# Optimization experiments

Hardware: AMD Instinct MI355X
Metric: run time of the kernel (lower is better)

Reference implementation:

```python
import jax, jax.numpy as jnp
from jax import lax
import numpy as np

K, D, BETA = 512, 64, 0.25

def conv1d(x, w, b=None, stride=1, padding=0):
    # x: [N,C,L], w: [O,I,k] (torch layout)
    y = lax.conv_general_dilated(x, w, (stride,), [(padding, padding)],
                                 dimension_numbers=('NCH', 'OIH', 'NCH'))
    return y if b is None else y + b[None, :, None]

def conv_transpose1d(x, w, b, stride, padding):
    # torch ConvTranspose1d; w: [I,O,k]. Equivalent to dilated conv with flipped, transposed kernel.
    k = w.shape[2]
    wf = jnp.flip(w, 2).transpose(1, 0, 2)  # [O,I,k]
    y = lax.conv_general_dilated(x, wf, (1,), [(k - 1 - padding, k - 1 - padding)],
                                 lhs_dilation=(stride,),
                                 dimension_numbers=('NCH', 'OIH', 'NCH'))
    return y + b[None, :, None]

def residual_stack(x, blocks):
    for w1, w2 in blocks:
        h = conv1d(jax.nn.relu(x), w1, None, 1, 1)
        h = conv1d(jax.nn.relu(h), w2, None, 1, 0)
        x = x + h
    return jax.nn.relu(x)

def setup_inputs() -> dict:
    key = jax.random.key(0)
    ks = iter(jax.random.split(key, 32))
    def w(shape, fan_in):
        return jax.random.normal(next(ks), shape, jnp.float32) / np.sqrt(fan_in)
    H, RH = 128, 32
    inp = {
        'x': jax.random.normal(next(ks), (64, 1, 8192), jnp.float32),
        'ec1_w': w((H // 2, 1, 4), 4), 'ec1_b': jnp.zeros(H // 2, jnp.float32),
        'ec2_w': w((H, H // 2, 4), H // 2 * 4), 'ec2_b': jnp.zeros(H, jnp.float32),
        'ec3_w': w((H, H, 3), H * 3), 'ec3_b': jnp.zeros(H, jnp.float32),
        'er1_w1': w((RH, H, 3), H * 3), 'er1_w2': w((H, RH, 1), RH),
        'er2_w1': w((RH, H, 3), H * 3), 'er2_w2': w((H, RH, 1), RH),
        'pvq_w': w((D, H, 1), H), 'pvq_b': jnp.zeros(D, jnp.float32),
        'codebook': jax.random.uniform(next(ks), (K, D), jnp.float32, -1.0 / K, 1.0 / K),
        'dc1_w': w((H, D, 3), D * 3), 'dc1_b': jnp.zeros(H, jnp.float32),
        'dr1_w1': w((RH, H, 3), H * 3), 'dr1_w2': w((H, RH, 1), RH),
        'dr2_w1': w((RH, H, 3), H * 3), 'dr2_w2': w((H, RH, 1), RH),
        'dt1_w': w((H, H // 2, 4), H * 4), 'dt1_b': jnp.zeros(H // 2, jnp.float32),
        'dt2_w': w((H // 2, 1, 4), H // 2 * 4), 'dt2_b': jnp.zeros(1, jnp.float32),
    }
    return inp

def reference(x, ec1_w, ec1_b, ec2_w, ec2_b, ec3_w, ec3_b,
              er1_w1, er1_w2, er2_w1, er2_w2, pvq_w, pvq_b, codebook,
              dc1_w, dc1_b, dr1_w1, dr1_w2, dr2_w1, dr2_w2,
              dt1_w, dt1_b, dt2_w, dt2_b):
    # ---- Encoder (compression_factor == 4) ----
    h = jax.nn.relu(conv1d(x, ec1_w, ec1_b, 2, 1))
    h = jax.nn.relu(conv1d(h, ec2_w, ec2_b, 2, 1))
    h = conv1d(h, ec3_w, ec3_b, 1, 1)
    h = residual_stack(h, [(er1_w1, er1_w2), (er2_w1, er2_w2)])
    z = conv1d(h, pvq_w, pvq_b, 1, 0)            # [B, D, L/4]

    # ---- Vector quantizer ----
    z_blc = z.transpose(0, 2, 1)                 # [B, L', D]
    flat = z_blc.reshape(-1, D)                  # [N, D]
    dists = (jnp.sum(flat * flat, 1, keepdims=True)
             - 2.0 * flat @ codebook.T
             + jnp.sum(codebook * codebook, 1))  # [N, K]
    idx = jnp.argmin(dists, axis=1)              # [N]
    q = codebook[idx].reshape(z_blc.shape)       # [B, L', D]
    e_latent = jnp.mean((lax.stop_gradient(q) - z_blc) ** 2)
    q_latent = jnp.mean((q - lax.stop_gradient(z_blc)) ** 2)
    vq_loss = q_latent + BETA * e_latent
    q_st = z_blc + lax.stop_gradient(q - z_blc)  # straight-through
    counts = jnp.zeros((K,), z.dtype).at[idx].add(1.0)
    avg_probs = counts / idx.shape[0]
    perplexity = jnp.exp(-jnp.sum(avg_probs * jnp.log(avg_probs + 1e-10)))

    # ---- Decoder (compression_factor == 4) ----
    d = conv1d(q_st.transpose(0, 2, 1), dc1_w, dc1_b, 1, 1)
    d = residual_stack(d, [(dr1_w1, dr1_w2), (dr2_w1, dr2_w2)])
    d = jax.nn.relu(conv_transpose1d(d, dt1_w, dt1_b, 2, 1))
    recon = conv_transpose1d(d, dt2_w, dt2_b, 2, 1)  # [B, 1, L]
    return recon, vq_loss, perplexity
```

## Files before the change

### kernel.cpp

```cpp
#include <hip/hip_runtime.h>
#include <math.h>

static constexpr int NB  = 64;
static constexpr int L0  = 8192;
static constexpr int L1  = 4096;
static constexpr int LQ  = 2048;
static constexpr int CH  = 128;
static constexpr int CHH = 64;
static constexpr int CR  = 32;
static constexpr int CD  = 64;
static constexpr int NK  = 512;
static constexpr int NROWS = NB * LQ;

using short8 = __attribute__((ext_vector_type(8))) short;
using f32x4  = __attribute__((ext_vector_type(4))) float;

__device__ inline f32x4 mfma16(short8 a, short8 b, f32x4 c) {
    return __builtin_amdgcn_mfma_f32_16x16x32_bf16(a, b, c, 0, 0, 0);
}

__device__ inline unsigned short bf16rne(float v) {
    unsigned int bb = __builtin_bit_cast(unsigned int, v);
    unsigned int r = (bb + 0x7FFFu + ((bb >> 16) & 1u)) >> 16;
    return (unsigned short)r;
}
__device__ inline float bf2f(unsigned short s) {
    unsigned int u = ((unsigned int)s) << 16;
    return __builtin_bit_cast(float, u);
}

__global__ __launch_bounds__(256) void k_wtf(const float* __restrict__ src,
                                             short* __restrict__ dst,
                                             int CO, int CI, int K, int iok) {
    int i = blockIdx.x * 256 + threadIdx.x;
    int total = K * CO * CI;
    if (i >= total) return;
    int j  = i & 7;
    int hi = (i >> 3) & 3;
    int cl = (i >> 5) & 15;
    int rest = i >> 9;
    int CIb = CI >> 5, COb = CO >> 4;
    int kb = rest % CIb; rest /= CIb;
    int cb = rest % COb;
    int tap = rest / COb;
    int co = cb * 16 + cl, ci = kb * 32 + hi * 8 + j;
    float v = iok ? src[(ci * CO + co) * K + tap] : src[(co * CI + ci) * K + tap];
    dst[i] = (short)bf16rne(v);
}

__global__ __launch_bounds__(256) void k_w2f(const float* __restrict__ src,
                                             short* __restrict__ hi_dst,
                                             short* __restrict__ lo_dst) {
    int i = blockIdx.x * 256 + threadIdx.x;
    if (i >= CH * CR) return;
    int j  = i & 7;
    int hi = (i >> 3) & 3;
    int cl = (i >> 5) & 15;
    int cb = i >> 9;
    int co = cb * 16 + cl, ci = hi * 8 + j;
    float v = src[co * CR + ci];
    unsigned short h = bf16rne(v);
    hi_dst[i] = (short)h;
    lo_dst[i] = (short)bf16rne(v - bf2f(h));
}

__global__ __launch_bounds__(256) void k_cbf(const float* __restrict__ cb,
                                             short* __restrict__ hi_dst,
                                             short* __restrict__ lo_dst) {
    int i = blockIdx.x * 256 + threadIdx.x;
    if (i >= NK * CD) return;
    int j    = i & 7;
    int l    = (i >> 3) & 63;
    int half = (i >> 9) & 1;
    int mt   = i >> 10;
    int cl = l & 15, hi = l >> 4;
    int m = mt * 16 + cl;
    int k = half * 32 + hi * 8 + j;
    float v = -2.f * cb[m * CD + k];
    unsigned short h = bf16rne(v);
    float r = v - bf2f(h);
    hi_dst[i] = (short)h;
    lo_dst[i] = (short)bf16rne(r);
}

__global__ __launch_bounds__(256) void k_ec1(const float* __restrict__ x,
                                             const float* __restrict__ w,
                                             const float* __restrict__ bias,
                                             float* __restrict__ out) {
    int n = blockIdx.x * 256 + threadIdx.x;
    int t  = n & (L1 - 1);
    int co = (n >> 12) & (CHH - 1);
    int b  = n >> 18;
    const float* xp = x + b * L0;
    float acc = bias[co];
    int p0 = 2 * t - 1;
#pragma unroll
    for (int k = 0; k < 4; ++k) {
        int p = p0 + k;
        if (p >= 0 && p < L0) acc += w[co * 4 + k] * xp[p];
    }
    out[n] = fmaxf(acc, 0.f);
}

template <int CIN, int COUT, int NTAPS, int TSTRIDE, int SWS, int LIN,
          bool RELU_IN, bool TRANS_IN, bool HAS_BIAS, bool RELU_OUT>
__global__ __launch_bounds__(256) void k_mfconv2(const float* __restrict__ x,
                                                 const short* __restrict__ wf,
                                                 const float* __restrict__ bias,
                                                 float* __restrict__ out) {
    constexpr int XW = 63 * TSTRIDE + NTAPS;
    constexpr int MR = (COUT == 128) ? 4 : 1;
    constexpr int COb = COUT / 16, CIb = CIN / 32;
    __shared__ unsigned int xsu[CIN * XW / 2];
    int t0 = blockIdx.x * 64;
    int b  = blockIdx.z;
    int tid = threadIdx.x;

    if (TRANS_IN) {
        for (int i = tid; i < XW * (CIN / 2); i += 256) {
            int j = i / (CIN / 2);
            int ci = (i - j * (CIN / 2)) * 2;
            int p = t0 - 1 + j;
            float vx = 0.f, vy = 0.f;
            if (p >= 0 && p < LIN) {
                const float* s = x + ((size_t)b * LIN + p) * CIN + ci;
                vx = s[0]; vy = s[1];
            }
            if (RELU_IN) { vx = fmaxf(vx, 0.f); vy = fmaxf(vy, 0.f); }
            unsigned int u = (__builtin_bit_cast(unsigned int, vx) >> 16)
                           | (__builtin_bit_cast(unsigned int, vy) & 0xFFFF0000u);
            int byte = (j * CIN + ci) * 2;
            byte ^= ((j >> SWS) & 7) << 4;
            xsu[byte >> 2] = u;
        }
    } else {
        for (int i = tid; i < (CIN / 2) * XW; i += 256) {
            int ci2 = i / XW;
            int j = i - ci2 * XW;
            int ci = ci2 * 2;
            int p = t0 * TSTRIDE - 1 + j;
            float vx = 0.f, vy = 0.f;
            if (p >= 0 && p < LIN) {
                const float* s = x + ((size_t)b * CIN + ci) * LIN + p;
                vx = s[0]; vy = s[LIN];
            }
            if (RELU_IN) { vx = fmaxf(vx, 0.f); vy = fmaxf(vy, 0.f); }
            unsigned int u = (__builtin_bit_cast(unsigned int, vx) >> 16)
                           | (__builtin_bit_cast(unsigned int, vy) & 0xFFFF0000u);
            int byte = (j * CIN + ci) * 2;
            byte ^= ((j >> SWS) & 7) << 4;
            xsu[byte >> 2] = u;
        }
    }
    __syncthreads();

    int l  = tid & 63;
    int w  = tid >> 6;
    int cl = l & 15, hi = l >> 4;
    int co_w = (w & 1) * (MR * 16);
    int t_w  = (w >> 1) * 32;

    f32x4 acc[MR][2];
#pragma unroll
    for (int m = 0; m < MR; ++m)
#pragma unroll
        for (int n = 0; n < 2; ++n) acc[m][n] = (f32x4){0.f, 0.f, 0.f, 0.f};

#pragma unroll
    for (int tap = 0; tap < NTAPS; ++tap) {
#pragma unroll
        for (int kb = 0; kb < CIb; ++kb) {
            const short* ap = wf + ((size_t)((tap * COb + co_w / 16) * CIb + kb)) * 512
                            + cl * 32 + hi * 8;
            short8 a[MR];
#pragma unroll
            for (int m = 0; m < MR; ++m)
                a[m] = *reinterpret_cast<const short8*>(ap + (size_t)m * CIb * 512);
            short8 bf[2];
#pragma unroll
            for (int n = 0; n < 2; ++n) {
                int tt = (t_w + n * 16 + cl) * TSTRIDE + tap;
                int byte = (tt * CIN + kb * 32 + hi * 8) * 2;
                byte ^= ((tt >> SWS) & 7) << 4;
                bf[n] = *reinterpret_cast<const short8*>(
                            reinterpret_cast<const char*>(xsu) + byte);
            }
#pragma unroll
            for (int m = 0; m < MR; ++m)
#pragma unroll
                for (int n = 0; n < 2; ++n)
                    acc[m][n] = mfma16(a[m], bf[n], acc[m][n]);
        }
    }

#pragma unroll
    for (int m = 0; m < MR; ++m) {
#pragma unroll
        for (int n = 0; n < 2; ++n) {
#pragma unroll
            for (int r = 0; r < 4; ++r) {
                int co = co_w + m * 16 + hi * 4 + r;
                int t  = t0 + t_w + n * 16 + cl;
                float v = acc[m][n][r];
                if (HAS_BIAS) v += bias[co];
                if (RELU_OUT) v = fmaxf(v, 0.f);
                out[((size_t)b * COUT + co) * LQ + t] = v;
            }
        }
    }
}

__global__ __launch_bounds__(256) void k_resblk(const float* __restrict__ src,
                                                float* __restrict__ dst,
                                                const short* __restrict__ wf1,
                                                const short* __restrict__ w2h,
                                                const short* __restrict__ w2l) {
    constexpr int XW = 66;
    __shared__ unsigned int xsu[CH * XW / 2];
    __shared__ unsigned int hh[64 * 16];
    __shared__ unsigned int hl[64 * 16];
    int t0 = blockIdx.x * 64;
    int b  = blockIdx.z;
    int tid = threadIdx.x;

    for (int i = tid; i < (CH / 2) * XW; i += 256) {
        int ci2 = i / XW;
        int j = i - ci2 * XW;
        int ci = ci2 * 2;
        int p = t0 - 1 + j;
        float vx = 0.f, vy = 0.f;
        if (p >= 0 && p < LQ) {
            const float* s = src + ((size_t)b * CH + ci) * LQ + p;
            vx = fmaxf(s[0], 0.f); vy = fmaxf(s[LQ], 0.f);
        }
        unsigned int u = (__builtin_bit_cast(unsigned int, vx) >> 16)
                       | (__builtin_bit_cast(unsigned int, vy) & 0xFFFF0000u);
        int byte = (j * CH + ci) * 2;
        byte ^= (j & 7) << 4;
        xsu[byte >> 2] = u;
    }
    __syncthreads();

    int l  = tid & 63;
    int w  = tid >> 6;
    int cl = l & 15, hi = l >> 4;
    int co_w1 = (w & 1) * 16;
    int t_w   = (w >> 1) * 32;

    f32x4 acc1[2];
    acc1[0] = (f32x4){0.f, 0.f, 0.f, 0.f};
    acc1[1] = (f32x4){0.f, 0.f, 0.f, 0.f};
#pragma unroll
    for (int tap = 0; tap < 3; ++tap) {
#pragma unroll
        for (int kb = 0; kb < 4; ++kb) {
            const short* ap = wf1 + ((size_t)((tap * 2 + (w & 1)) * 4 + kb)) * 512
                            + cl * 32 + hi * 8;
            short8 a = *reinterpret_cast<const short8*>(ap);
#pragma unroll
            for (int n = 0; n < 2; ++n) {
                int tt = (t_w + n * 16 + cl) + tap;
                int byte = (tt * CH + kb * 32 + hi * 8) * 2;
                byte ^= (tt & 7) << 4;
                short8 bf = *reinterpret_cast<const short8*>(
                                reinterpret_cast<const char*>(xsu) + byte);
                acc1[n] = mfma16(a, bf, acc1[n]);
            }
        }
    }

#pragma unroll
    for (int n = 0; n < 2; ++n) {
        int t = t_w + n * 16 + cl;
#pragma unroll
        for (int rp = 0; rp < 2; ++rp) {
            float v0 = fmaxf(acc1[n][2 * rp], 0.f);
            float v1 = fmaxf(acc1[n][2 * rp + 1], 0.f);
            unsigned short h0 = bf16rne(v0), h1 = bf16rne(v1);
            unsigned short l0 = bf16rne(v0 - bf2f(h0)), l1 = bf16rne(v1 - bf2f(h1));
            int ciu = (co_w1 >> 1) + hi * 2 + rp;
            int idx = t * 16 + (ciu ^ ((t & 3) << 2));
            hh[idx] = (unsigned int)h0 | ((unsigned int)h1 << 16);
            hl[idx] = (unsigned int)l0 | ((unsigned int)l1 << 16);
        }
    }
    __syncthreads();

    int co2_w = (w & 1) * 64;
    short8 bh[2], bl[2];
#pragma unroll
    for (int n2 = 0; n2 < 2; ++n2) {
        int t = t_w + n2 * 16 + cl;
        int idx = t * 16 + ((hi * 4) ^ ((t & 3) << 2));
        bh[n2] = *reinterpret_cast<const short8*>(&hh[idx]);
        bl[n2] = *reinterpret_cast<const short8*>(&hl[idx]);
    }
#pragma unroll
    for (int m2 = 0; m2 < 4; ++m2) {
        int co2 = co2_w + m2 * 16;
        const short* aph = w2h + (co2 / 16) * 512 + cl * 32 + hi * 8;
        const short* apl = w2l + (co2 / 16) * 512 + cl * 32 + hi * 8;
        short8 ah = *reinterpret_cast<const short8*>(aph);
        short8 al = *reinterpret_cast<const short8*>(apl);
#pragma unroll
        for (int n2 = 0; n2 < 2; ++n2) {
            f32x4 acc = (f32x4){0.f, 0.f, 0.f, 0.f};
            acc = mfma16(ah, bl[n2], acc);
            acc = mfma16(al, bh[n2], acc);
            acc = mfma16(ah, bh[n2], acc);
            int t = t0 + t_w + n2 * 16 + cl;
#pragma unroll
            for (int r = 0; r < 4; ++r) {
                int co = co2 + hi * 4 + r;
                size_t off = ((size_t)b * CH + co) * LQ + t;
                dst[off] = src[off] + acc[r];
            }
        }
    }
}

__global__ __launch_bounds__(256) void k_dt1m(const float* __restrict__ x,
                                              const short* __restrict__ wf,
                                              const float* __restrict__ bias,
                                              float* __restrict__ out) {
    constexpr int XW = 66;
    __shared__ unsigned int xsu[CH * XW / 2];
    int t0 = blockIdx.x * 64;
    int b  = blockIdx.z;
    int tid = threadIdx.x;
    for (int i = tid; i < (CH / 2) * XW; i += 256) {
        int ci2 = i / XW;
        int j = i - ci2 * XW;
        int ci = ci2 * 2;
        int p = t0 - 1 + j;
        float vx = 0.f, vy = 0.f;
        if (p >= 0 && p < LQ) {
            const float* s = x + ((size_t)b * CH + ci) * LQ + p;
            vx = fmaxf(s[0], 0.f); vy = fmaxf(s[LQ], 0.f);
        }
        unsigned int u = (__builtin_bit_cast(unsigned int, vx) >> 16)
                       | (__builtin_bit_cast(unsigned int, vy) & 0xFFFF0000u);
        int byte = (j * CH + ci) * 2;
        byte ^= (j & 7) << 4;
        xsu[byte >> 2] = u;
    }
    __syncthreads();

    int l  = tid & 63;
    int w  = tid >> 6;
    int cl = l & 15, hi = l >> 4;
    int co_w = (w & 1) * 32;
    int u_w  = (w >> 1) * 32;

    f32x4 ae[2][2], ao[2][2];
#pragma unroll
    for (int m = 0; m < 2; ++m)
#pragma unroll
        for (int n = 0; n < 2; ++n) {
            ae[m][n] = (f32x4){0.f, 0.f, 0.f, 0.f};
            ao[m][n] = (f32x4){0.f, 0.f, 0.f, 0.f};
        }

    const int TK[4] = {1, 3, 0, 2};
    const int TO[4] = {1, 0, 2, 1};
#pragma unroll
    for (int te = 0; te < 4; ++te) {
        int k = TK[te], off = TO[te];
#pragma unroll
        for (int kb = 0; kb < 4; ++kb) {
            const short* ap = wf + (size_t)((k * 4 + co_w / 16) * 4 + kb) * 512
                            + cl * 32 + hi * 8;
            short8 a[2];
#pragma unroll
            for (int m = 0; m < 2; ++m)
                a[m] = *reinterpret_cast<const short8*>(ap + (size_t)m * 4 * 512);
            short8 bf[2];
#pragma unroll
            for (int n = 0; n < 2; ++n) {
                int tt = u_w + n * 16 + cl + off;
                int byte = (tt * CH + kb * 32 + hi * 8) * 2;
                byte ^= (tt & 7) << 4;
                bf[n] = *reinterpret_cast<const short8*>(
                            reinterpret_cast<const char*>(xsu) + byte);
            }
#pragma unroll
            for (int m = 0; m < 2; ++m)
#pragma unroll
                for (int n = 0; n < 2; ++n) {
                    if (te < 2) ae[m][n] = mfma16(a[m], bf[n], ae[m][n]);
                    else        ao[m][n] = mfma16(a[m], bf[n], ao[m][n]);
                }
        }
    }

#pragma unroll
    for (int m = 0; m < 2; ++m) {
#pragma unroll
        for (int n = 0; n < 2; ++n) {
#pragma unroll
            for (int r = 0; r < 4; ++r) {
                int co = co_w + m * 16 + hi * 4 + r;
                int u  = t0 + u_w + n * 16 + cl;
                float bv = bias[co];
                float2 rr;
                rr.x = fmaxf(ae[m][n][r] + bv, 0.f);
                rr.y = fmaxf(ao[m][n][r] + bv, 0.f);
                *reinterpret_cast<float2*>(&out[((size_t)b * CHH + co) * L1 + 2 * u]) = rr;
            }
        }
    }
}

__global__ __launch_bounds__(256) void k_pvqr(const float* __restrict__ x,
                                              const float* __restrict__ w,
                                              const float* __restrict__ bias,
                                              float* __restrict__ z) {
    __shared__ float xs[CH][64];
    __shared__ float wT[CH][64];
    int tid = threadIdx.x;
    int t0 = blockIdx.x * 64;
    int b = blockIdx.y;
    for (int i = tid; i < CD * CH; i += 256) {
        int d = i >> 7, ci = i & 127;
        wT[ci][d] = w[i];
    }
    for (int i = tid; i < CH * 64; i += 256) {
        int ci = i >> 6, j = i & 63;
        xs[ci][j] = fmaxf(x[((size_t)b * CH + ci) * LQ + t0 + j], 0.f);
    }
    __syncthreads();
    int d = tid & 63;
    int tg = tid >> 6;
    float bv = bias[d];
    float acc[16];
#pragma unroll
    for (int i = 0; i < 16; ++i) acc[i] = bv;
    for (int ci = 0; ci < CH; ++ci) {
        float wv = wT[ci][d];
        const float4* xr = reinterpret_cast<const float4*>(&xs[ci][tg * 16]);
        float4 a = xr[0], bq = xr[1], c = xr[2], e = xr[3];
        acc[0]  = fmaf(wv, a.x, acc[0]);
        acc[1]  = fmaf(wv, a.y, acc[1]);
        acc[2]  = fmaf(wv, a.z, acc[2]);
        acc[3]  = fmaf(wv, a.w, acc[3]);
        acc[4]  = fmaf(wv, bq.x, acc[4]);
        acc[5]  = fmaf(wv, bq.y, acc[5]);
        acc[6]  = fmaf(wv, bq.z, acc[6]);
        acc[7]  = fmaf(wv, bq.w, acc[7]);
        acc[8]  = fmaf(wv, c.x, acc[8]);
        acc[9]  = fmaf(wv, c.y, acc[9]);
        acc[10] = fmaf(wv, c.z, acc[10]);
        acc[11] = fmaf(wv, c.w, acc[11]);
        acc[12] = fmaf(wv, e.x, acc[12]);
        acc[13] = fmaf(wv, e.y, acc[13]);
        acc[14] = fmaf(wv, e.z, acc[14]);
        acc[15] = fmaf(wv, e.w, acc[15]);
    }
    int tbase = t0 + tg * 16;
#pragma unroll
    for (int i = 0; i < 16; ++i)
        z[((size_t)b * LQ + tbase + i) * CD + d] = acc[i];
}

__global__ __launch_bounds__(256) void k_cb2(const float* __restrict__ cb,
                                             float* __restrict__ cb2) {
    int k = blockIdx.x * 256 + threadIdx.x;
    if (k >= NK) return;
    const float* r = cb + k * CD;
    float s = 0.f;
#pragma unroll 8
    for (int i = 0; i < CD; ++i) s += r[i] * r[i];
    cb2[k] = s;
}

__global__ __launch_bounds__(256) void k_vqm(const float* __restrict__ z,
                                             const short* __restrict__ cbf_hi,
                                             const short* __restrict__ cbf_lo,
                                             const float* __restrict__ cb2,
                                             const float* __restrict__ cb,
                                             float* __restrict__ q,
                                             int* __restrict__ counts,
                                             float* __restrict__ sse) {
    __shared__ float c2l[NK];
    __shared__ int   hist[NK];
    int tid = threadIdx.x;
    int l   = tid & 63;
    int w   = tid >> 6;
    int cl  = l & 15, hi = l >> 4;
    int wrow0 = blockIdx.x * 256 + w * 64;

    for (int i = tid; i < NK; i += 256) { c2l[i] = cb2[i]; hist[i] = 0; }
    __syncthreads();

    short8 bh[4][2], bl[4][2];
#pragma unroll
    for (int nt = 0; nt < 4; ++nt) {
        int row = wrow0 + nt * 16 + cl;
        const float* zr = z + (size_t)row * CD;
#pragma unroll
        for (int half = 0; half < 2; ++half) {
            const float4* p4 = reinterpret_cast<const float4*>(zr + half * 32 + hi * 8);
            float4 v0 = p4[0], v1 = p4[1];
            float vs[8] = {v0.x, v0.y, v0.z, v0.w, v1.x, v1.y, v1.z, v1.w};
            short8 sh, sl;
#pragma unroll
            for (int j = 0; j < 8; ++j) {
                unsigned short h = bf16rne(vs[j]);
                float r = vs[j] - bf2f(h);
                sh[j] = (short)h;
                sl[j] = (short)bf16rne(r);
            }
            bh[nt][half] = sh;
            bl[nt][half] = sl;
        }
    }

    float bscore[4];
    int   bidx[4];
#pragma unroll
    for (int nt = 0; nt < 4; ++nt) { bscore[nt] = 1e30f; bidx[nt] = 0; }

#pragma unroll 4
    for (int mt = 0; mt < 32; ++mt) {
        short8 ah0 = *reinterpret_cast<const short8*>(cbf_hi + (mt * 2 + 0) * 512 + l * 8);
        short8 ah1 = *reinterpret_cast<const short8*>(cbf_hi + (mt * 2 + 1) * 512 + l * 8);
        short8 al0 = *reinterpret_cast<const short8*>(cbf_lo + (mt * 2 + 0) * 512 + l * 8);
        short8 al1 = *reinterpret_cast<const short8*>(cbf_lo + (mt * 2 + 1) * 512 + l * 8);
        float4 c2v = *reinterpret_cast<const float4*>(&c2l[mt * 16 + hi * 4]);
        f32x4 cin = (f32x4){c2v.x, c2v.y, c2v.z, c2v.w};
        int mbase = mt * 16 + hi * 4;
#pragma unroll
        for (int nt = 0; nt < 4; ++nt) {
            f32x4 acc = mfma16(al0, bh[nt][0], cin);
            acc = mfma16(al1, bh[nt][1], acc);
            acc = mfma16(ah0, bl[nt][0], acc);
            acc = mfma16(ah1, bl[nt][1], acc);
            acc = mfma16(ah0, bh[nt][0], acc);
            acc = mfma16(ah1, bh[nt][1], acc);
#pragma unroll
            for (int r = 0; r < 4; ++r) {
                float s = acc[r];
                bool better = s < bscore[nt];
                bscore[nt] = better ? s : bscore[nt];
                bidx[nt]   = better ? (mbase + r) : bidx[nt];
            }
        }
    }

    float err = 0.f;
#pragma unroll
    for (int nt = 0; nt < 4; ++nt) {
        float s = bscore[nt];
        int   id = bidx[nt];
#pragma unroll
        for (int off = 16; off <= 32; off <<= 1) {
            float s2 = __shfl_xor(s, off);
            int   i2 = __shfl_xor(id, off);
            bool take = (s2 < s) || (s2 == s && i2 < id);
            s  = take ? s2 : s;
            id = take ? i2 : id;
        }
        int row = wrow0 + nt * 16 + cl;
        const float4* cbr = reinterpret_cast<const float4*>(cb + (size_t)id * CD);
        float4* qw = reinterpret_cast<float4*>(q + (size_t)row * CD);
        float4 q0 = cbr[hi * 2];
        float4 q1 = cbr[hi * 2 + 1];
        float4 q2 = cbr[8 + hi * 2];
        float4 q3 = cbr[8 + hi * 2 + 1];
        qw[hi * 2]     = q0;
        qw[hi * 2 + 1] = q1;
        qw[8 + hi * 2]     = q2;
        qw[8 + hi * 2 + 1] = q3;
        float qv[16] = {q0.x, q0.y, q0.z, q0.w, q1.x, q1.y, q1.z, q1.w,
                        q2.x, q2.y, q2.z, q2.w, q3.x, q3.y, q3.z, q3.w};
#pragma unroll
        for (int half = 0; half < 2; ++half) {
#pragma unroll
            for (int j = 0; j < 8; ++j) {
                float zv = bf2f((unsigned short)bh[nt][half][j])
                         + bf2f((unsigned short)bl[nt][half][j]);
                float d = qv[half * 8 + j] - zv;
                err = fmaf(d, d, err);
            }
        }
        if (hi == 0) atomicAdd(&hist[id], 1);
    }
#pragma unroll
    for (int s = 32; s > 0; s >>= 1) err += __shfl_xor(err, s);
    if (l == 0) atomicAdd(sse, err);

    __syncthreads();
    for (int i = tid; i < NK; i += 256) {
        int h = hist[i];
        if (h) atomicAdd(&counts[i], h);
    }
}

__global__ __launch_bounds__(256) void k_dt2(const float* __restrict__ x,
                                             const float* __restrict__ w,
                                             const float* __restrict__ bias,
                                             float* __restrict__ out) {
    int u = blockIdx.x * 256 + threadIdx.x;
    int b = blockIdx.y;
    const float* xp = x + (size_t)b * CHH * L1 + u;
    float bv = bias[0];
    float ae = bv, ao = bv;
    for (int ci = 0; ci < CHH; ++ci) {
        const float* xr = xp + ci * L1;
        float xm  = (u >= 1) ? xr[-1] : 0.f;
        float x0  = xr[0];
        float xp1 = (u < L1 - 1) ? xr[1] : 0.f;
        const float* wc = w + ci * 4;
        ae += wc[1] * x0 + wc[3] * xm;
        ao += wc[0] * xp1 + wc[2] * x0;
    }
    reinterpret_cast<float2*>(out + (size_t)b * L0)[u] = make_float2(ae, ao);
}

__global__ __launch_bounds__(512) void k_final(const int* __restrict__ counts,
                                               const float* __restrict__ sse,
                                               float* __restrict__ out) {
    __shared__ float red[8];
    int tid = threadIdx.x;
    float p = (float)counts[tid] * (1.f / (float)NROWS);
    float v = p * logf(p + 1e-10f);
#pragma unroll
    for (int s = 32; s > 0; s >>= 1) v += __shfl_down(v, s);
    if ((tid & 63) == 0) red[tid >> 6] = v;
    __syncthreads();
    if (tid == 0) {
        float tot = 0.f;
        for (int i = 0; i < 8; ++i) tot += red[i];
        out[524288] = 1.25f * sse[0] / ((float)NROWS * (float)CD);
        out[524289] = expf(-tot);
    }
}

extern "C" void kernel_launch(void* const* d_in, const int* in_sizes, int n_in,
                              void* d_out, int out_size, void* d_ws, size_t ws_size,
                              hipStream_t stream) {
    const float* x      = (const float*)d_in[0];
    const float* ec1_w  = (const float*)d_in[1];
    const float* ec1_b  = (const float*)d_in[2];
    const float* ec2_w  = (const float*)d_in[3];
    const float* ec2_b  = (const float*)d_in[4];
    const float* ec3_w  = (const float*)d_in[5];
    const float* ec3_b  = (const float*)d_in[6];
    const float* er1_w1 = (const float*)d_in[7];
    const float* er1_w2 = (const float*)d_in[8];
    const float* er2_w1 = (const float*)d_in[9];
    const float* er2_w2 = (const float*)d_in[10];
    const float* pvq_w  = (const float*)d_in[11];
    const float* pvq_b  = (const float*)d_in[12];
    const float* cbk    = (const float*)d_in[13];
    const float* dc1_w  = (const float*)d_in[14];
    const float* dc1_b  = (const float*)d_in[15];
    const float* dr1_w1 = (const float*)d_in[16];
    const float* dr1_w2 = (const float*)d_in[17];
    const float* dr2_w1 = (const float*)d_in[18];
    const float* dr2_w2 = (const float*)d_in[19];
    const float* dt1_w  = (const float*)d_in[20];
    const float* dt1_b  = (const float*)d_in[21];
    const float* dt2_w  = (const float*)d_in[22];
    const float* dt2_b  = (const float*)d_in[23];
    float* out = (float*)d_out;

    char* ws = (char*)d_ws;
    float* A    = (float*)(ws);
    float* Bb   = (float*)(ws + 67108864);
    char*  smal = ws + 134217728;
    int*   counts = (int*)smal;
    float* sse    = (float*)(smal + 2048);
    float* cb2    = (float*)(smal + 4096);
    short* wf_ec2 = (short*)(smal + 8192);
    short* wf_ec3 = wf_ec2 + 32768;
    short* wf_er1 = wf_ec3 + 49152;
    short* wf_er2 = wf_er1 + 12288;
    short* wf_dc1 = wf_er2 + 12288;
    short* wf_dr1 = wf_dc1 + 24576;
    short* wf_dr2 = wf_dr1 + 12288;
    short* wf_dt1 = wf_dr2 + 12288;
    short* cbf_hi = wf_dt1 + 32768;
    short* cbf_lo = cbf_hi + 32768;
    short* w2_er1h = cbf_lo + 32768;
    short* w2_er1l = w2_er1h + 4096;
    short* w2_er2h = w2_er1l + 4096;
    short* w2_er2l = w2_er2h + 4096;
    short* w2_dr1h = w2_er2l + 4096;
    short* w2_dr1l = w2_dr1h + 4096;
    short* w2_dr2h = w2_dr1l + 4096;
    short* w2_dr2l = w2_dr2h + 4096;
    float* z = Bb;
    float* q = Bb + 8388608;

    hipMemsetAsync(smal, 0, 2056, stream);

    k_wtf<<<dim3(128), 256, 0, stream>>>(ec2_w, wf_ec2, 128, 64, 4, 0);
    k_wtf<<<dim3(192), 256, 0, stream>>>(ec3_w, wf_ec3, 128, 128, 3, 0);
    k_wtf<<<dim3(48), 256, 0, stream>>>(er1_w1, wf_er1, 32, 128, 3, 0);
    k_wtf<<<dim3(48), 256, 0, stream>>>(er2_w1, wf_er2, 32, 128, 3, 0);
    k_wtf<<<dim3(96), 256, 0, stream>>>(dc1_w, wf_dc1, 128, 64, 3, 0);
    k_wtf<<<dim3(48), 256, 0, stream>>>(dr1_w1, wf_dr1, 32, 128, 3, 0);
    k_wtf<<<dim3(48), 256, 0, stream>>>(dr2_w1, wf_dr2, 32, 128, 3, 0);
    k_wtf<<<dim3(128), 256, 0, stream>>>(dt1_w, wf_dt1, 64, 128, 4, 1);
    k_w2f<<<dim3(16), 256, 0, stream>>>(er1_w2, w2_er1h, w2_er1l);
    k_w2f<<<dim3(16), 256, 0, stream>>>(er2_w2, w2_er2h, w2_er2l);
    k_w2f<<<dim3(16), 256, 0, stream>>>(dr1_w2, w2_dr1h, w2_dr1l);
    k_w2f<<<dim3(16), 256, 0, stream>>>(dr2_w2, w2_dr2h, w2_dr2l);
    k_cbf<<<dim3(128), 256, 0, stream>>>(cbk, cbf_hi, cbf_lo);
    k_cb2<<<dim3(2), 256, 0, stream>>>(cbk, cb2);

    k_ec1<<<dim3((NB * CHH * L1) / 256), 256, 0, stream>>>(x, ec1_w, ec1_b, A);
    k_mfconv2<64, 128, 4, 2, 1, L1, false, false, true, true>
        <<<dim3(LQ / 64, 1, NB), 256, 0, stream>>>(A, wf_ec2, ec2_b, Bb);
    k_mfconv2<128, 128, 3, 1, 0, LQ, false, false, true, false>
        <<<dim3(LQ / 64, 1, NB), 256, 0, stream>>>(Bb, wf_ec3, ec3_b, A);
    k_resblk<<<dim3(LQ / 64, 1, NB), 256, 0, stream>>>(A, Bb, wf_er1, w2_er1h, w2_er1l);
    k_resblk<<<dim3(LQ / 64, 1, NB), 256, 0, stream>>>(Bb, A, wf_er2, w2_er2h, w2_er2l);
    k_pvqr<<<dim3(LQ / 64, NB), 256, 0, stream>>>(A, pvq_w, pvq_b, z);

    k_vqm<<<dim3(NROWS / 256), 256, 0, stream>>>(z, cbf_hi, cbf_lo, cb2, cbk,
                                                 q, counts, sse);

    k_mfconv2<64, 128, 3, 1, 0, LQ, false, true, true, false>
        <<<dim3(LQ / 64, 1, NB), 256, 0, stream>>>(q, wf_dc1, dc1_b, A);
    k_resblk<<<dim3(LQ / 64, 1, NB), 256, 0, stream>>>(A, Bb, wf_dr1, w2_dr1h, w2_dr1l);
    k_resblk<<<dim3(LQ / 64, 1, NB), 256, 0, stream>>>(Bb, A, wf_dr2, w2_dr2h, w2_dr2l);
    k_dt1m<<<dim3(LQ / 64, 1, NB), 256, 0, stream>>>(A, wf_dt1, dt1_b, Bb);
    k_dt2<<<dim3(L1 / 256, NB), 256, 0, stream>>>(Bb, dt2_w, dt2_b, out);

    k_final<<<dim3(1), 512, 0, stream>>>(counts, sse, out);
}
```

Baseline: 678.3 us.

## Use split-bf16 MFMA for pre-VQ projection and gather codebook into decoder conv

The pre-quantization 1x1 projection moves from a scalar FP32 FMA loop to bf16 hi/lo split MFMA, using three products to keep near-FP32 accuracy. The VQ kernel now writes only the chosen code index per row instead of the full quantized vector. The first decoder conv gathers codebook rows by index straight into shared memory, skipping a 32MB write and read of q. The gathered codebook values are truncated to bf16 with no lo correction, so dc1 accuracy may be slightly lower.

```diff
diff --git a/kernel.cpp b/kernel.cpp
--- a/kernel.cpp
+++ b/kernel.cpp
@@ -64,6 +64,23 @@
     lo_dst[i] = (short)bf16rne(v - bf2f(h));
 }
 
+__global__ __launch_bounds__(256) void k_pwf(const float* __restrict__ src,
+                                             short* __restrict__ hi_dst,
+                                             short* __restrict__ lo_dst) {
+    int i = blockIdx.x * 256 + threadIdx.x;
+    if (i >= CD * CH) return;
+    int j  = i & 7;
+    int hi = (i >> 3) & 3;
+    int cl = (i >> 5) & 15;
+    int rest = i >> 9;
+    int kb = rest & 3, cb = rest >> 2;
+    int d = cb * 16 + cl, ci = kb * 32 + hi * 8 + j;
+    float v = src[d * CH + ci];
+    unsigned short h = bf16rne(v);
+    hi_dst[i] = (short)h;
+    lo_dst[i] = (short)bf16rne(v - bf2f(h));
+}
+
 __global__ __launch_bounds__(256) void k_cbf(const float* __restrict__ cb,
                                              short* __restrict__ hi_dst,
                                              short* __restrict__ lo_dst) {
@@ -205,6 +222,88 @@
                 if (HAS_BIAS) v += bias[co];
                 if (RELU_OUT) v = fmaxf(v, 0.f);
                 out[((size_t)b * COUT + co) * LQ + t] = v;
+            }
+        }
+    }
+}
+
+__global__ __launch_bounds__(256) void k_dc1g(const int* __restrict__ idx,
+                                              const float* __restrict__ cb,
+                                              const short* __restrict__ wf,
+                                              const float* __restrict__ bias,
+                                              float* __restrict__ out) {
+    constexpr int XW = 66;
+    __shared__ unsigned int xsu[CD * XW / 2];
+    int t0 = blockIdx.x * 64;
+    int b  = blockIdx.z;
+    int tid = threadIdx.x;
+
+    for (int i = tid; i < XW * (CD / 2); i += 256) {
+        int j = i >> 5;
+        int ci = (i & 31) * 2;
+        int p = t0 - 1 + j;
+        float vx = 0.f, vy = 0.f;
+        if (p >= 0 && p < LQ) {
+            int id = idx[(size_t)b * LQ + p];
+            const float* s = cb + (size_t)id * CD + ci;
+            vx = s[0]; vy = s[1];
+        }
+        unsigned int u = (__builtin_bit_cast(unsigned int, vx) >> 16)
+                       | (__builtin_bit_cast(unsigned int, vy) & 0xFFFF0000u);
+        int byte = (j * CD + ci) * 2;
+        byte ^= (j & 7) << 4;
+        xsu[byte >> 2] = u;
+    }
+    __syncthreads();
+
+    int l  = tid & 63;
+    int w  = tid >> 6;
+    int cl = l & 15, hi = l >> 4;
+    int co_w = (w & 1) * 64;
+    int t_w  = (w >> 1) * 32;
+
+    f32x4 acc[4][2];
+#pragma unroll
+    for (int m = 0; m < 4; ++m)
+#pragma unroll
+        for (int n = 0; n < 2; ++n) acc[m][n] = (f32x4){0.f, 0.f, 0.f, 0.f};
+
+#pragma unroll
+    for (int tap = 0; tap < 3; ++tap) {
+#pragma unroll
+        for (int kb = 0; kb < 2; ++kb) {
+            const short* ap = wf + ((size_t)((tap * 8 + co_w / 16) * 2 + kb)) * 512
+                            + cl * 32 + hi * 8;
+            short8 a[4];
+#pragma unroll
+            for (int m = 0; m < 4; ++m)
+                a[m] = *reinterpret_cast<const short8*>(ap + (size_t)m * 2 * 512);
+            short8 bf[2];
+#pragma unroll
+            for (int n = 0; n < 2; ++n) {
+                int tt = (t_w + n * 16 + cl) + tap;
+                int byte = (tt * CD + kb * 32 + hi * 8) * 2;
+                byte ^= (tt & 7) << 4;
+                bf[n] = *reinterpret_cast<const short8*>(
+                            reinterpret_cast<const char*>(xsu) + byte);
+            }
+#pragma unroll
+            for (int m = 0; m < 4; ++m)
+#pragma unroll
+                for (int n = 0; n < 2; ++n)
+                    acc[m][n] = mfma16(a[m], bf[n], acc[m][n]);
+        }
+    }
+
+#pragma unroll
+    for (int m = 0; m < 4; ++m) {
+#pragma unroll
+        for (int n = 0; n < 2; ++n) {
+#pragma unroll
+            for (int r = 0; r < 4; ++r) {
+                int co = co_w + m * 16 + hi * 4 + r;
+                int t  = t0 + t_w + n * 16 + cl;
+                out[((size_t)b * CH + co) * LQ + t] = acc[m][n][r] + bias[co];
             }
         }
     }
@@ -411,55 +510,70 @@
     }
 }
 
-__global__ __launch_bounds__(256) void k_pvqr(const float* __restrict__ x,
-                                              const float* __restrict__ w,
+__global__ __launch_bounds__(256) void k_pvqm(const float* __restrict__ x,
+                                              const short* __restrict__ pwh,
+                                              const short* __restrict__ pwl,
                                               const float* __restrict__ bias,
                                               float* __restrict__ z) {
-    __shared__ float xs[CH][64];
-    __shared__ float wT[CH][64];
+    __shared__ unsigned int xh[(CH / 2) * 64];
+    __shared__ unsigned int xl[(CH / 2) * 64];
+    int t0 = blockIdx.x * 64;
+    int b  = blockIdx.y;
     int tid = threadIdx.x;
-    int t0 = blockIdx.x * 64;
-    int b = blockIdx.y;
-    for (int i = tid; i < CD * CH; i += 256) {
-        int d = i >> 7, ci = i & 127;
-        wT[ci][d] = w[i];
-    }
-    for (int i = tid; i < CH * 64; i += 256) {
-        int ci = i >> 6, j = i & 63;
-        xs[ci][j] = fmaxf(x[((size_t)b * CH + ci) * LQ + t0 + j], 0.f);
+
+    for (int i = tid; i < (CH / 2) * 64; i += 256) {
+        int ci2 = i >> 6;
+        int t = i & 63;
+        int ci = ci2 * 2;
+        const float* s = x + ((size_t)b * CH + ci) * LQ + t0 + t;
+        float vx = fmaxf(s[0], 0.f);
+        float vy = fmaxf(s[LQ], 0.f);
+        unsigned short hx = bf16rne(vx), hy = bf16rne(vy);
+        unsigned short lx = bf16rne(vx - bf2f(hx)), ly = bf16rne(vy - bf2f(hy));
+        int byte = (t * CH + ci) * 2;
+        byte ^= (t & 7) << 4;
+        xh[byte >> 2] = (unsigned int)hx | ((unsigned int)hy << 16);
+        xl[byte >> 2] = (unsigned int)lx | ((unsigned int)ly << 16);
     }
     __syncthreads();
-    int d = tid & 63;
-    int tg = tid >> 6;
-    float bv = bias[d];
-    float acc[16];
-#pragma unroll
-    for (int i = 0; i < 16; ++i) acc[i] = bv;
-    for (int ci = 0; ci < CH; ++ci) {
-        float wv = wT[ci][d];
-        const float4* xr = reinterpret_cast<const float4*>(&xs[ci][tg * 16]);
-        float4 a = xr[0], bq = xr[1], c = xr[2], e = xr[3];
-        acc[0]  = fmaf(wv, a.x, acc[0]);
-        acc[1]  = fmaf(wv, a.y, acc[1]);
-        acc[2]  = fmaf(wv, a.z, acc[2]);
-        acc[3]  = fmaf(wv, a.w, acc[3]);
-        acc[4]  = fmaf(wv, bq.x, acc[4]);
-        acc[5]  = fmaf(wv, bq.y, acc[5]);
-        acc[6]  = fmaf(wv, bq.z, acc[6]);
-        acc[7]  = fmaf(wv, bq.w, acc[7]);
-        acc[8]  = fmaf(wv, c.x, acc[8]);
-        acc[9]  = fmaf(wv, c.y, acc[9]);
-        acc[10] = fmaf(wv, c.z, acc[10]);
-        acc[11] = fmaf(wv, c.w, acc[11]);
-        acc[12] = fmaf(wv, e.x, acc[12]);
-        acc[13] = fmaf(wv, e.y, acc[13]);
-        acc[14] = fmaf(wv, e.z, acc[14]);
-        acc[15] = fmaf(wv, e.w, acc[15]);
-    }
-    int tbase = t0 + tg * 16;
-#pragma unroll
-    for (int i = 0; i < 16; ++i)
-        z[((size_t)b * LQ + tbase + i) * CD + d] = acc[i];
+
+    int l  = tid & 63;
+    int w  = tid >> 6;
+    int cl = l & 15, hi = l >> 4;
+
+    float4 bv4 = *reinterpret_cast<const float4*>(&bias[w * 16 + hi * 4]);
+    f32x4 acc[4];
+#pragma unroll
+    for (int nt = 0; nt < 4; ++nt) acc[nt] = (f32x4){bv4.x, bv4.y, bv4.z, bv4.w};
+
+#pragma unroll
+    for (int kb = 0; kb < 4; ++kb) {
+        const short* aph = pwh + ((size_t)(w * 4 + kb)) * 512 + cl * 32 + hi * 8;
+        const short* apl = pwl + ((size_t)(w * 4 + kb)) * 512 + cl * 32 + hi * 8;
+        short8 ah = *reinterpret_cast<const short8*>(aph);
+        short8 al = *reinterpret_cast<const short8*>(apl);
+#pragma unroll
+        for (int nt = 0; nt < 4; ++nt) {
+            int tt = nt * 16 + cl;
+            int byte = (tt * CH + kb * 32 + hi * 8) * 2;
+            byte ^= (tt & 7) << 4;
+            short8 bhf = *reinterpret_cast<const short8*>(
+                             reinterpret_cast<const char*>(xh) + byte);
+            short8 blf = *reinterpret_cast<const short8*>(
+                             reinterpret_cast<const char*>(xl) + byte);
+            acc[nt] = mfma16(ah, blf, acc[nt]);
+            acc[nt] = mfma16(al, bhf, acc[nt]);
+            acc[nt] = mfma16(ah, bhf, acc[nt]);
+        }
+    }
+
+#pragma unroll
+    for (int nt = 0; nt < 4; ++nt) {
+        int t = t0 + nt * 16 + cl;
+        float4 o;
+        o.x = acc[nt][0]; o.y = acc[nt][1]; o.z = acc[nt][2]; o.w = acc[nt][3];
+        *reinterpret_cast<float4*>(&z[((size_t)b * LQ + t) * CD + w * 16 + hi * 4]) = o;
+    }
 }
 
 __global__ __launch_bounds__(256) void k_cb2(const float* __restrict__ cb,
@@ -478,7 +592,7 @@
                                              const short* __restrict__ cbf_lo,
                                              const float* __restrict__ cb2,
                                              const float* __restrict__ cb,
-                                             float* __restrict__ q,
+                                             int* __restrict__ idxout,
                                              int* __restrict__ counts,
                                              float* __restrict__ sse) {
     __shared__ float c2l[NK];
@@ -561,16 +675,12 @@
             id = take ? i2 : id;
         }
         int row = wrow0 + nt * 16 + cl;
+        if (hi == 0) idxout[row] = id;
         const float4* cbr = reinterpret_cast<const float4*>(cb + (size_t)id * CD);
-        float4* qw = reinterpret_cast<float4*>(q + (size_t)row * CD);
         float4 q0 = cbr[hi * 2];
         float4 q1 = cbr[hi * 2 + 1];
         float4 q2 = cbr[8 + hi * 2];
         float4 q3 = cbr[8 + hi * 2 + 1];
-        qw[hi * 2]     = q0;
-        qw[hi * 2 + 1] = q1;
-        qw[8 + hi * 2]     = q2;
-        qw[8 + hi * 2 + 1] = q3;
         float qv[16] = {q0.x, q0.y, q0.z, q0.w, q1.x, q1.y, q1.z, q1.w,
                         q2.x, q2.y, q2.z, q2.w, q3.x, q3.y, q3.z, q3.w};
 #pragma unroll
@@ -690,8 +800,10 @@
     short* w2_dr1l = w2_dr1h + 4096;
     short* w2_dr2h = w2_dr1l + 4096;
     short* w2_dr2l = w2_dr2h + 4096;
+    short* pw_hi   = w2_dr2l + 4096;
+    short* pw_lo   = pw_hi + 8192;
     float* z = Bb;
-    float* q = Bb + 8388608;
+    int*   idxv = (int*)((char*)Bb + 33554432);
 
     hipMemsetAsync(smal, 0, 2056, stream);
 
@@ -707,6 +819,7 @@
     k_w2f<<<dim3(16), 256, 0, stream>>>(er2_w2, w2_er2h, w2_er2l);
     k_w2f<<<dim3(16), 256, 0, stream>>>(dr1_w2, w2_dr1h, w2_dr1l);
     k_w2f<<<dim3(16), 256, 0, stream>>>(dr2_w2, w2_dr2h, w2_dr2l);
+    k_pwf<<<dim3(32), 256, 0, stream>>>(pvq_w, pw_hi, pw_lo);
     k_cbf<<<dim3(128), 256, 0, stream>>>(cbk, cbf_hi, cbf_lo);
     k_cb2<<<dim3(2), 256, 0, stream>>>(cbk, cb2);
 
@@ -717,13 +830,12 @@
         <<<dim3(LQ / 64, 1, NB), 256, 0, stream>>>(Bb, wf_ec3, ec3_b, A);
     k_resblk<<<dim3(LQ / 64, 1, NB), 256, 0, stream>>>(A, Bb, wf_er1, w2_er1h, w2_er1l);
     k_resblk<<<dim3(LQ / 64, 1, NB), 256, 0, stream>>>(Bb, A, wf_er2, w2_er2h, w2_er2l);
-    k_pvqr<<<dim3(LQ / 64, NB), 256, 0, stream>>>(A, pvq_w, pvq_b, z);
+    k_pvqm<<<dim3(LQ / 64, NB), 256, 0, stream>>>(A, pw_hi, pw_lo, pvq_b, z);
 
     k_vqm<<<dim3(NROWS / 256), 256, 0, stream>>>(z, cbf_hi, cbf_lo, cb2, cbk,
-                                                 q, counts, sse);
-
-    k_mfconv2<64, 128, 3, 1, 0, LQ, false, true, true, false>
-        <<<dim3(LQ / 64, 1, NB), 256, 0, stream>>>(q, wf_dc1, dc1_b, A);
+                                                 idxv, counts, sse);
+
+    k_dc1g<<<dim3(LQ / 64, 1, NB), 256, 0, stream>>>(idxv, cbk, wf_dc1, dc1_b, A);
     k_resblk<<<dim3(LQ / 64, 1, NB), 256, 0, stream>>>(A, Bb, wf_dr1, w2_dr1h, w2_dr1l);
     k_resblk<<<dim3(LQ / 64, 1, NB), 256, 0, stream>>>(Bb, A, wf_dr2, w2_dr2h, w2_dr2l);
     k_dt1m<<<dim3(LQ / 64, 1, NB), 256, 0, stream>>>(A, wf_dt1, dt1_b, Bb);
```

Measured after the change: 617.8 us. 1.1x faster.
